# Kernel optimization log

Hardware: AMD Instinct MI355X
Metric: run time of the kernel (lower is better)

The kernel has to match this reference:

```python
import jax, jax.numpy as jnp
import numpy as np

DEFAULT_MASK_VALUE = -0.7 * float(np.finfo(np.float32).max)

B, S, HQ, HKV, D = 2, 2048, 16, 8, 128
CHUNK = 512


def _chunk_causal_mask(seq_len, chunk_size):
    # True where attention allowed: same chunk AND causal within chunk.
    row = jax.lax.broadcasted_iota(jnp.int32, (seq_len, seq_len), 0)
    col = jax.lax.broadcasted_iota(jnp.int32, (seq_len, seq_len), 1)
    return (row // chunk_size == col // chunk_size) & (row >= col)


def _block_mask_indices(bidirectional_mask):
    # [B, L] 0/1 -> segment ids, e.g. [0,1,1,1,0,0,1,1,0,1,0] -> [0,1,1,1,0,0,2,2,0,3,0]
    m = bidirectional_mask.astype(jnp.int32)
    padded = jnp.pad(m, [(0, 0), (1, 0)], constant_values=0)
    boundary = padded[..., 1:] > padded[..., :-1]
    return m * jnp.cumsum(boundary, axis=-1)


def _bidirectional_block_mask(bidirectional_mask):
    idx = _block_mask_indices(bidirectional_mask)  # [B, L]
    return (idx[:, None, :] == idx[:, :, None]) & (idx[:, :, None] > 0)  # [B, L, L]


def setup_inputs() -> dict:
    key = jax.random.key(0)
    kq, kk, kv, kb = jax.random.split(key, 4)
    q = jax.random.normal(kq, (B, S, HQ, D), dtype=jnp.float32)
    k = jax.random.normal(kk, (B, S, HKV, D), dtype=jnp.float32)
    v = jax.random.normal(kv, (B, S, HKV, D), dtype=jnp.float32)
    bidirectional_mask = jax.random.randint(kb, (B, S), 0, 2, dtype=jnp.int32)
    return {"q": q, "k": k, "v": v, "bidirectional_mask": bidirectional_mask,
            "chunk_size": CHUNK}


def reference(q, k, v, bidirectional_mask, chunk_size):
    b, s, hq, d = q.shape
    hkv = k.shape[2]
    group = hq // hkv  # GQA group size
    scale = 1.0 / jnp.sqrt(jnp.asarray(d, q.dtype))

    # [b, s, hkv, group, d]
    qg = q.reshape(b, s, hkv, group, d) * scale
    # logits: [b, hkv, group, q, kv]
    logits = jnp.einsum("bqhgd,bkhd->bhgqk", qg, k)

    # combined mask: chunked-causal OR bidirectional block (image tokens attend
    # bidirectionally within their contiguous block)
    chunk_mask = _chunk_causal_mask(s, chunk_size)                 # [s, s]
    bidir_mask = _bidirectional_block_mask(bidirectional_mask)    # [b, s, s]
    allowed = chunk_mask[None, :, :] | bidir_mask                  # [b, s, s]
    allowed = allowed[:, None, None, :, :]                         # [b, 1, 1, s, s]

    masked = jnp.where(allowed, logits, DEFAULT_MASK_VALUE)
    probs = jax.nn.softmax(masked, axis=-1)

    out = jnp.einsum("bhgqk,bkhd->bqhgd", probs, v)
    return out.reshape(b, s, hq, d)
```

## Files before the change

kernel.cpp:

```cpp
#include <hip/hip_runtime.h>
#include <hip/hip_bf16.h>

#define SLEN 2048
#define BATCH 2
#define NHQ 16
#define NHKV 8
#define DIM 128
#define SEG 512
#define NSEG (SLEN / SEG)

#define KTD (64 * 64)
#define VTD (128 * 32)

typedef __attribute__((ext_vector_type(8))) short bf16x8;
typedef __attribute__((ext_vector_type(4))) short bf16x4;
typedef __attribute__((ext_vector_type(4))) float f32x4;

static __device__ inline short f2bf(float f) {
    __hip_bfloat16 h = __float2bfloat16(f);
    return *reinterpret_cast<short*>(&h);
}
static __device__ inline unsigned pack_bf2(float lo, float hi) {
    unsigned a = (unsigned)(unsigned short)f2bf(lo);
    unsigned b = (unsigned)(unsigned short)f2bf(hi);
    return a | (b << 16);
}
static __device__ inline float fast_exp2(float x) {
#if __has_builtin(__builtin_amdgcn_exp2f)
    return __builtin_amdgcn_exp2f(x);
#else
    return __builtin_exp2f(x);
#endif
}
static __device__ inline f32x4 mfma16(bf16x4 a, bf16x4 b, f32x4 c) {
#if __has_builtin(__builtin_amdgcn_mfma_f32_16x16x16bf16_1k)
    return __builtin_amdgcn_mfma_f32_16x16x16bf16_1k(a, b, c, 0, 0, 0);
#else
    asm volatile("v_mfma_f32_16x16x16_bf16 %0, %1, %2, %0\n\ts_nop 7\n\ts_nop 7"
                 : "+v"(c) : "v"(a), "v"(b));
    return c;
#endif
}

#define GLDS(g, l) __builtin_amdgcn_global_load_lds( \
    (const __attribute__((address_space(1))) void*)(g), \
    (__attribute__((address_space(3))) void*)(l), 16, 0, 0)

__global__ __launch_bounds__(256) void conv_kv(
    const float* __restrict__ K, const float* __restrict__ V,
    unsigned short* __restrict__ Kb, unsigned short* __restrict__ Vt,
    const int* __restrict__ mask, int* __restrict__ rs, int* __restrict__ re)
{
    __shared__ float vt_s[64 * 132];
    __shared__ int   sm[SLEN];
    const int blk = blockIdx.x;
    const int NCONV = BATCH * NHKV * (SLEN / 64);

    if (blk >= NCONV) {
        const int idx = blk - NCONV;
        const int b = idx >> 3, slice = idx & 7;
        const int* mb = mask + b * SLEN;
        for (int i = threadIdx.x; i < SLEN; i += 256) sm[i] = mb[i];
        __syncthreads();
        const int i = slice * 256 + threadIdx.x;
        int s0 = -1, e0 = -2;
        if (sm[i] == 1) {
            s0 = i; while (s0 > 0 && sm[s0 - 1] == 1) --s0;
            e0 = i; while (e0 < SLEN - 1 && sm[e0 + 1] == 1) ++e0;
        }
        rs[b * SLEN + i] = s0;
        re[b * SLEN + i] = e0;
        return;
    }

    const int st = blk & 31;
    const int h  = (blk >> 5) & 7;
    const int b  = blk >> 8;
    const int s0 = st * 64;
    const int sl = threadIdx.x >> 2;
    const int dq = (threadIdx.x & 3) * 32;

    {
        const float* ksrc = K + (((size_t)(b * SLEN + s0 + sl) * NHKV + h) * DIM) + dq;
        unsigned short* kdst = Kb + (((size_t)(b * NHKV + h) * SLEN) + s0 + sl) * DIM + dq;
        #pragma unroll
        for (int i = 0; i < 4; ++i) {
            float4 a = ((const float4*)ksrc)[2 * i];
            float4 c = ((const float4*)ksrc)[2 * i + 1];
            ((uint4*)kdst)[i] = make_uint4(pack_bf2(a.x, a.y), pack_bf2(a.z, a.w),
                                           pack_bf2(c.x, c.y), pack_bf2(c.z, c.w));
        }
    }

    {
        const float* vsrc = V + (((size_t)(b * SLEN + s0 + sl) * NHKV + h) * DIM) + dq;
        float4* ld = (float4*)&vt_s[sl * 132 + dq];
        #pragma unroll
        for (int i = 0; i < 8; ++i) ld[i] = ((const float4*)vsrc)[i];
    }
    __syncthreads();
    #pragma unroll
    for (int pass = 0; pass < 2; ++pass) {
        const int dl = (threadIdx.x >> 2) + pass * 64;
        const int sw = (threadIdx.x & 3) * 16;
        unsigned pk[8];
        #pragma unroll
        for (int m = 0; m < 8; ++m)
            pk[m] = pack_bf2(vt_s[(sw + 2 * m) * 132 + dl],
                             vt_s[(sw + 2 * m + 1) * 132 + dl]);
        unsigned short* dst = Vt + (((size_t)(b * NHKV + h) * DIM) + dl) * SLEN + s0 + sw;
        ((uint4*)dst)[0] = make_uint4(pk[0], pk[1], pk[2], pk[3]);
        ((uint4*)dst)[1] = make_uint4(pk[4], pk[5], pk[6], pk[7]);
    }
}

__global__ __launch_bounds__(512, 2) void attn_fwd(
    const float* __restrict__ Q, const unsigned short* __restrict__ KbP,
    const unsigned short* __restrict__ VtP, const int* __restrict__ rs,
    const int* __restrict__ re, const int* __restrict__ csp,
    float* __restrict__ Out)
{
    const int tid  = threadIdx.x;
    const int wid  = tid >> 6;
    const int lane = tid & 63;
    const int quad = lane >> 4;
    const int n    = lane & 15;

    const int bid   = blockIdx.x;
    const int h     = bid & 7;
    const int inner = (bid >> 3) & 15;
    const int q4    = (bid >> 7) & 3;
    const int band  = (q4 == 0) ? 3 : (q4 == 1) ? 2 : (q4 == 2) ? 0 : 1;
    const int b     = inner & 1;
    const int hq    = h * 2 + ((inner >> 1) & 1);
    const int chunk = inner >> 2;
    const int r0 = chunk * SEG + band * 128 + wid * 16;

    __shared__ unsigned pool[2 * KTD + 2 * VTD];

    const float scale = 0.08838834764831845f * 1.4426950408889634f;
    const int cs = csp[0];

    const int* rsb = rs + b * SLEN;
    const int* reb = re + b * SLEN;

    const int row  = r0 + n;
    const int rsvq = rsb[row];
    const int csrq = (row / cs) * cs;
    int lo_rt, hi_rt;
    {
        const int revq = reb[row];
        int lo = csrq; if (rsvq >= 0 && rsvq < lo) lo = rsvq;
        int hi = row;  if (revq > hi) hi = revq;
        #pragma unroll
        for (int off = 8; off > 0; off >>= 1) {
            lo = min(lo, __shfl_xor(lo, off, 64));
            hi = max(hi, __shfl_xor(hi, off, 64));
        }
        lo_rt = lo; hi_rt = hi;
    }
    const int cshi = ((r0 + 15) / cs) * cs;

    bf16x8 qa[4];
    {
        const float* qp = Q + (((size_t)(b * SLEN + row) * NHQ + hq) * DIM) + quad * 8;
        #pragma unroll
        for (int kb = 0; kb < 4; ++kb) {
            float4 f0 = *(const float4*)(qp + kb * 32);
            float4 f1 = *(const float4*)(qp + kb * 32 + 4);
            bf16x8 a;
            a[0] = f2bf(f0.x * scale); a[1] = f2bf(f0.y * scale);
            a[2] = f2bf(f0.z * scale); a[3] = f2bf(f0.w * scale);
            a[4] = f2bf(f1.x * scale); a[5] = f2bf(f1.y * scale);
            a[6] = f2bf(f1.z * scale); a[7] = f2bf(f1.w * scale);
            qa[kb] = a;
        }
    }

    int lo_blk, hi_blk;
    {
        int* sred = (int*)pool;
        if (lane == 0) { sred[wid * 2] = lo_rt; sred[wid * 2 + 1] = hi_rt; }
        __syncthreads();
        int lo = 0x7fffffff, hi = 0;
        #pragma unroll
        for (int i = 0; i < 8; ++i) {
            lo = min(lo, sred[2 * i]);
            hi = max(hi, sred[2 * i + 1]);
        }
        __syncthreads();
        lo_blk = lo & ~63;
        hi_blk = hi;
    }

    float lrow = 0.0f;
    f32x4 o[8];
    #pragma unroll
    for (int nb = 0; nb < 8; ++nb) o[nb] = (f32x4){0.f, 0.f, 0.f, 0.f};

    const unsigned short* KbB = KbP + (size_t)(b * NHKV + h) * SLEN * DIM;
    const unsigned short* VtB = VtP + (size_t)(b * NHKV + h) * DIM * SLEN;

    const int kr0  = tid >> 4;
    const int ksl  = (tid & 15) ^ (kr0 & 15);
    const size_t koff = (size_t)kr0 * DIM + ksl * 8;
    const int vr0  = tid >> 3;
    const int vsl  = (tid & 7) ^ (vr0 & 7);
    const size_t voff = (size_t)vr0 * SLEN + vsl * 8;

    int rsv_c;
    {
        const unsigned short* ks = KbB + (size_t)lo_blk * DIM + koff;
        const unsigned short* vs = VtB + lo_blk + voff;
        char* kl = (char*)pool;
        char* vl = (char*)pool + 32768;
        GLDS(ks,                     kl + tid * 16);
        GLDS(ks + (size_t)32 * DIM,  kl + 8192 + tid * 16);
        GLDS(vs,                     vl + tid * 16);
        GLDS(vs + (size_t)64 * SLEN, vl + 8192 + tid * 16);
        rsv_c = rsb[lo_blk + lane];
    }
    __syncthreads();

    int bufi = 0;
    for (int k0 = lo_blk; k0 <= hi_blk; k0 += 64, bufi ^= 1) {
        int rsv_n = rsv_c;
        if (k0 + 64 <= hi_blk) {
            const int kn0 = k0 + 64;
            const unsigned short* ks = KbB + (size_t)kn0 * DIM + koff;
            const unsigned short* vs = VtB + kn0 + voff;
            char* kl = (char*)pool + (bufi ^ 1) * 16384;
            char* vl = (char*)pool + 32768 + (bufi ^ 1) * 16384;
            GLDS(ks,                     kl + tid * 16);
            GLDS(ks + (size_t)32 * DIM,  kl + 8192 + tid * 16);
            GLDS(vs,                     vl + tid * 16);
            GLDS(vs + (size_t)64 * SLEN, vl + 8192 + tid * 16);
            rsv_n = rsb[kn0 + lane];
        }

        if ((k0 + 63 >= lo_rt) && (k0 <= hi_rt)) {
            const short* ktb = (const short*)(pool + bufi * KTD);
            const short* vtb = (const short*)(pool + 2 * KTD + bufi * VTD);

            f32x4 sfr[4];
            #pragma unroll
            for (int c = 0; c < 4; ++c) sfr[c] = (f32x4){0.f, 0.f, 0.f, 0.f};
            __builtin_amdgcn_s_setprio(1);
            #pragma unroll
            for (int c = 0; c < 4; ++c) {
                #pragma unroll
                for (int kb = 0; kb < 4; ++kb) {
                    const bf16x8 kf = *(const bf16x8*)(ktb +
                        (c * 16 + n) * DIM + (((kb * 4 + quad) ^ n) * 8));
                    sfr[c] = __builtin_amdgcn_mfma_f32_16x16x32_bf16(kf, qa[kb], sfr[c], 0, 0, 0);
                }
            }
            __builtin_amdgcn_s_setprio(0);

            const bool fullc = (k0 >= cshi) && (k0 + 63 <= r0);
            if (!fullc) {
                #pragma unroll
                for (int c = 0; c < 4; ++c) {
                    #pragma unroll
                    for (int g = 0; g < 4; ++g) {
                        const int kcl  = k0 + c * 16 + quad * 4 + g;
                        const int rskv = __shfl(rsv_c, c * 16 + quad * 4 + g, 64);
                        const bool ok = ((kcl >= csrq) && (kcl <= row)) ||
                                        (rsvq >= 0 && rskv == rsvq);
                        if (!ok) sfr[c][g] = -3.0e38f;
                    }
                }
            }

            bf16x4 pa[4];
            #pragma unroll
            for (int c = 0; c < 4; ++c) {
                float p0 = fast_exp2(sfr[c][0]);
                float p1 = fast_exp2(sfr[c][1]);
                float p2 = fast_exp2(sfr[c][2]);
                float p3 = fast_exp2(sfr[c][3]);
                lrow += (p0 + p1) + (p2 + p3);
                uint2 ww = make_uint2(pack_bf2(p0, p1), pack_bf2(p2, p3));
                pa[c] = __builtin_bit_cast(bf16x4, ww);
            }

            __builtin_amdgcn_s_setprio(1);
            #pragma unroll
            for (int c = 0; c < 4; ++c) {
                #pragma unroll
                for (int nb = 0; nb < 8; ++nb) {
                    const bf16x4 vb = *(const bf16x4*)(vtb +
                        (nb * 16 + n) * 64 + (((c * 2 + (quad >> 1)) ^ (n & 7)) * 8)
                        + (quad & 1) * 4);
                    o[nb] = mfma16(pa[c], vb, o[nb]);
                }
            }
            __builtin_amdgcn_s_setprio(0);
        }

        __syncthreads();
        rsv_c = rsv_n;
    }

    lrow += __shfl_xor(lrow, 16, 64);
    lrow += __shfl_xor(lrow, 32, 64);
    const float inv = 1.0f / lrow;
    #pragma unroll
    for (int g = 0; g < 4; ++g) {
        const float invg = __shfl(inv, quad * 4 + g, 64);
        const int r = r0 + quad * 4 + g;
        float* op = Out + ((size_t)(b * SLEN + r) * NHQ + hq) * DIM + n;
        #pragma unroll
        for (int nb = 0; nb < 8; ++nb)
            op[nb * 16] = o[nb][g] * invg;
    }
}

extern "C" void kernel_launch(void* const* d_in, const int* in_sizes, int n_in,
                              void* d_out, int out_size, void* d_ws, size_t ws_size,
                              hipStream_t stream) {
    const float* q  = (const float*)d_in[0];
    const float* k  = (const float*)d_in[1];
    const float* v  = (const float*)d_in[2];
    const int*   bm = (const int*)d_in[3];
    const int*   cs = (const int*)d_in[4];
    float* out = (float*)d_out;

    int* rs = (int*)d_ws;
    int* re = rs + BATCH * SLEN;
    unsigned short* Kb = (unsigned short*)((char*)d_ws + 32768);
    unsigned short* Vt = Kb + (size_t)BATCH * NHKV * SLEN * DIM;

    hipLaunchKernelGGL(conv_kv, dim3(BATCH * NHKV * (SLEN / 64) + BATCH * 8), dim3(256),
                       0, stream, k, v, Kb, Vt, bm, rs, re);
    hipLaunchKernelGGL(attn_fwd, dim3(512), dim3(512), 0, stream,
                       q, Kb, Vt, rs, re, cs, out);
}
```

Before: 131.3 us.

## Process two 16-row query tiles per wave to reuse K/V fragments

Each wave now handles 32 query rows as two 16-row sub-tiles, so every K and V fragment read from LDS feeds two MFMAs. The block shrinks from 512 to 256 threads, and each thread issues four async global-to-LDS loads per tile instead of two. The aim is to halve LDS reads per MFMA and cut per-block overhead. The cost is roughly double the accumulator and Q registers, plus launch bounds of (256,1) that may lower occupancy and latency hiding.

```diff
diff --git a/kernel.cpp b/kernel.cpp
--- a/kernel.cpp
+++ b/kernel.cpp
@@ -114,7 +114,7 @@
     }
 }
 
-__global__ __launch_bounds__(512, 2) void attn_fwd(
+__global__ __launch_bounds__(256, 1) void attn_fwd(
     const float* __restrict__ Q, const unsigned short* __restrict__ KbP,
     const unsigned short* __restrict__ VtP, const int* __restrict__ rs,
     const int* __restrict__ re, const int* __restrict__ csp,
@@ -134,7 +134,7 @@
     const int b     = inner & 1;
     const int hq    = h * 2 + ((inner >> 1) & 1);
     const int chunk = inner >> 2;
-    const int r0 = chunk * SEG + band * 128 + wid * 16;
+    const int r0 = chunk * SEG + band * 128 + wid * 32;
 
     __shared__ unsigned pool[2 * KTD + 2 * VTD];
 
@@ -144,14 +144,20 @@
     const int* rsb = rs + b * SLEN;
     const int* reb = re + b * SLEN;
 
-    const int row  = r0 + n;
-    const int rsvq = rsb[row];
-    const int csrq = (row / cs) * cs;
+    const int row0 = r0 + n;
+    const int row1 = r0 + 16 + n;
+    const int rsv0 = rsb[row0];
+    const int rsv1 = rsb[row1];
+    const int csr0 = (row0 / cs) * cs;
+    const int csr1 = (row1 / cs) * cs;
     int lo_rt, hi_rt;
     {
-        const int revq = reb[row];
-        int lo = csrq; if (rsvq >= 0 && rsvq < lo) lo = rsvq;
-        int hi = row;  if (revq > hi) hi = revq;
+        const int rev0 = reb[row0];
+        const int rev1 = reb[row1];
+        int lo = min(csr0, csr1);
+        if (rsv0 >= 0) lo = min(lo, rsv0);
+        if (rsv1 >= 0) lo = min(lo, rsv1);
+        int hi = max(max(row1, rev0), rev1);
         #pragma unroll
         for (int off = 8; off > 0; off >>= 1) {
             lo = min(lo, __shfl_xor(lo, off, 64));
@@ -159,11 +165,13 @@
         }
         lo_rt = lo; hi_rt = hi;
     }
-    const int cshi = ((r0 + 15) / cs) * cs;
-
-    bf16x8 qa[4];
-    {
-        const float* qp = Q + (((size_t)(b * SLEN + row) * NHQ + hq) * DIM) + quad * 8;
+    const int cshi0 = ((r0 + 15) / cs) * cs;
+    const int cshi1 = ((r0 + 31) / cs) * cs;
+
+    bf16x8 qa[2][4];
+    #pragma unroll
+    for (int u = 0; u < 2; ++u) {
+        const float* qp = Q + (((size_t)(b * SLEN + r0 + 16 * u + n) * NHQ + hq) * DIM) + quad * 8;
         #pragma unroll
         for (int kb = 0; kb < 4; ++kb) {
             float4 f0 = *(const float4*)(qp + kb * 32);
@@ -173,7 +181,7 @@
             a[2] = f2bf(f0.z * scale); a[3] = f2bf(f0.w * scale);
             a[4] = f2bf(f1.x * scale); a[5] = f2bf(f1.y * scale);
             a[6] = f2bf(f1.z * scale); a[7] = f2bf(f1.w * scale);
-            qa[kb] = a;
+            qa[u][kb] = a;
         }
     }
 
@@ -184,7 +192,7 @@
         __syncthreads();
         int lo = 0x7fffffff, hi = 0;
         #pragma unroll
-        for (int i = 0; i < 8; ++i) {
+        for (int i = 0; i < 4; ++i) {
             lo = min(lo, sred[2 * i]);
             hi = max(hi, sred[2 * i + 1]);
         }
@@ -193,20 +201,20 @@
         hi_blk = hi;
     }
 
-    float lrow = 0.0f;
-    f32x4 o[8];
+    float lrow[2] = {0.f, 0.f};
+    f32x4 o[2][8];
     #pragma unroll
-    for (int nb = 0; nb < 8; ++nb) o[nb] = (f32x4){0.f, 0.f, 0.f, 0.f};
+    for (int u = 0; u < 2; ++u)
+        #pragma unroll
+        for (int nb = 0; nb < 8; ++nb) o[u][nb] = (f32x4){0.f, 0.f, 0.f, 0.f};
 
     const unsigned short* KbB = KbP + (size_t)(b * NHKV + h) * SLEN * DIM;
     const unsigned short* VtB = VtP + (size_t)(b * NHKV + h) * DIM * SLEN;
 
-    const int kr0  = tid >> 4;
-    const int ksl  = (tid & 15) ^ (kr0 & 15);
-    const size_t koff = (size_t)kr0 * DIM + ksl * 8;
-    const int vr0  = tid >> 3;
-    const int vsl  = (tid & 7) ^ (vr0 & 7);
-    const size_t voff = (size_t)vr0 * SLEN + vsl * 8;
+    const int ksl  = (tid & 15) ^ ((tid >> 4) & 15);
+    const size_t koff = (size_t)(tid >> 4) * DIM + ksl * 8;
+    const int vsl  = (tid & 7) ^ ((tid >> 3) & 7);
+    const size_t voff = (size_t)(tid >> 3) * SLEN + vsl * 8;
 
     int rsv_c;
     {
@@ -214,10 +222,11 @@
         const unsigned short* vs = VtB + lo_blk + voff;
         char* kl = (char*)pool;
         char* vl = (char*)pool + 32768;
-        GLDS(ks,                     kl + tid * 16);
-        GLDS(ks + (size_t)32 * DIM,  kl + 8192 + tid * 16);
-        GLDS(vs,                     vl + tid * 16);
-        GLDS(vs + (size_t)64 * SLEN, vl + 8192 + tid * 16);
+        #pragma unroll
+        for (int p = 0; p < 4; ++p) {
+            GLDS(ks + (size_t)(p * 16) * DIM,  kl + tid * 16 + p * 4096);
+            GLDS(vs + (size_t)(p * 32) * SLEN, vl + tid * 16 + p * 4096);
+        }
         rsv_c = rsb[lo_blk + lane];
     }
     __syncthreads();
@@ -231,10 +240,11 @@
             const unsigned short* vs = VtB + kn0 + voff;
             char* kl = (char*)pool + (bufi ^ 1) * 16384;
             char* vl = (char*)pool + 32768 + (bufi ^ 1) * 16384;
-            GLDS(ks,                     kl + tid * 16);
-            GLDS(ks + (size_t)32 * DIM,  kl + 8192 + tid * 16);
-            GLDS(vs,                     vl + tid * 16);
-            GLDS(vs + (size_t)64 * SLEN, vl + 8192 + tid * 16);
+            #pragma unroll
+            for (int p = 0; p < 4; ++p) {
+                GLDS(ks + (size_t)(p * 16) * DIM,  kl + tid * 16 + p * 4096);
+                GLDS(vs + (size_t)(p * 32) * SLEN, vl + tid * 16 + p * 4096);
+            }
             rsv_n = rsb[kn0 + lane];
         }
 
@@ -242,9 +252,11 @@
             const short* ktb = (const short*)(pool + bufi * KTD);
             const short* vtb = (const short*)(pool + 2 * KTD + bufi * VTD);
 
-            f32x4 sfr[4];
-            #pragma unroll
-            for (int c = 0; c < 4; ++c) sfr[c] = (f32x4){0.f, 0.f, 0.f, 0.f};
+            f32x4 sfr[2][4];
+            #pragma unroll
+            for (int u = 0; u < 2; ++u)
+                #pragma unroll
+                for (int c = 0; c < 4; ++c) sfr[u][c] = (f32x4){0.f, 0.f, 0.f, 0.f};
             __builtin_amdgcn_s_setprio(1);
             #pragma unroll
             for (int c = 0; c < 4; ++c) {
@@ -252,36 +264,48 @@
                 for (int kb = 0; kb < 4; ++kb) {
                     const bf16x8 kf = *(const bf16x8*)(ktb +
                         (c * 16 + n) * DIM + (((kb * 4 + quad) ^ n) * 8));
-                    sfr[c] = __builtin_amdgcn_mfma_f32_16x16x32_bf16(kf, qa[kb], sfr[c], 0, 0, 0);
+                    sfr[0][c] = __builtin_amdgcn_mfma_f32_16x16x32_bf16(kf, qa[0][kb], sfr[0][c], 0, 0, 0);
+                    sfr[1][c] = __builtin_amdgcn_mfma_f32_16x16x32_bf16(kf, qa[1][kb], sfr[1][c], 0, 0, 0);
                 }
             }
             __builtin_amdgcn_s_setprio(0);
 
-            const bool fullc = (k0 >= cshi) && (k0 + 63 <= r0);
-            if (!fullc) {
+            const bool f0 = (k0 >= cshi0) && (k0 + 63 <= r0);
+            const bool f1 = (k0 >= cshi1) && (k0 + 63 <= r0 + 16);
+            if (!(f0 && f1)) {
                 #pragma unroll
                 for (int c = 0; c < 4; ++c) {
                     #pragma unroll
                     for (int g = 0; g < 4; ++g) {
                         const int kcl  = k0 + c * 16 + quad * 4 + g;
                         const int rskv = __shfl(rsv_c, c * 16 + quad * 4 + g, 64);
-                        const bool ok = ((kcl >= csrq) && (kcl <= row)) ||
-                                        (rsvq >= 0 && rskv == rsvq);
-                        if (!ok) sfr[c][g] = -3.0e38f;
+                        if (!f0) {
+                            const bool ok = ((kcl >= csr0) && (kcl <= row0)) ||
+                                            (rsv0 >= 0 && rskv == rsv0);
+                            if (!ok) sfr[0][c][g] = -3.0e38f;
+                        }
+                        if (!f1) {
+                            const bool ok = ((kcl >= csr1) && (kcl <= row1)) ||
+                                            (rsv1 >= 0 && rskv == rsv1);
+                            if (!ok) sfr[1][c][g] = -3.0e38f;
+                        }
                     }
                 }
             }
 
-            bf16x4 pa[4];
-            #pragma unroll
-            for (int c = 0; c < 4; ++c) {
-                float p0 = fast_exp2(sfr[c][0]);
-                float p1 = fast_exp2(sfr[c][1]);
-                float p2 = fast_exp2(sfr[c][2]);
-                float p3 = fast_exp2(sfr[c][3]);
-                lrow += (p0 + p1) + (p2 + p3);
-                uint2 ww = make_uint2(pack_bf2(p0, p1), pack_bf2(p2, p3));
-                pa[c] = __builtin_bit_cast(bf16x4, ww);
+            bf16x4 pa[2][4];
+            #pragma unroll
+            for (int u = 0; u < 2; ++u) {
+                #pragma unroll
+                for (int c = 0; c < 4; ++c) {
+                    float p0 = fast_exp2(sfr[u][c][0]);
+                    float p1 = fast_exp2(sfr[u][c][1]);
+                    float p2 = fast_exp2(sfr[u][c][2]);
+                    float p3 = fast_exp2(sfr[u][c][3]);
+                    lrow[u] += (p0 + p1) + (p2 + p3);
+                    uint2 ww = make_uint2(pack_bf2(p0, p1), pack_bf2(p2, p3));
+                    pa[u][c] = __builtin_bit_cast(bf16x4, ww);
+                }
             }
 
             __builtin_amdgcn_s_setprio(1);
@@ -292,7 +316,8 @@
                     const bf16x4 vb = *(const bf16x4*)(vtb +
                         (nb * 16 + n) * 64 + (((c * 2 + (quad >> 1)) ^ (n & 7)) * 8)
                         + (quad & 1) * 4);
-                    o[nb] = mfma16(pa[c], vb, o[nb]);
+                    o[0][nb] = mfma16(pa[0][c], vb, o[0][nb]);
+                    o[1][nb] = mfma16(pa[1][c], vb, o[1][nb]);
                 }
             }
             __builtin_amdgcn_s_setprio(0);
@@ -302,17 +327,21 @@
         rsv_c = rsv_n;
     }
 
-    lrow += __shfl_xor(lrow, 16, 64);
-    lrow += __shfl_xor(lrow, 32, 64);
-    const float inv = 1.0f / lrow;
     #pragma unroll
-    for (int g = 0; g < 4; ++g) {
-        const float invg = __shfl(inv, quad * 4 + g, 64);
-        const int r = r0 + quad * 4 + g;
-        float* op = Out + ((size_t)(b * SLEN + r) * NHQ + hq) * DIM + n;
-        #pragma unroll
-        for (int nb = 0; nb < 8; ++nb)
-            op[nb * 16] = o[nb][g] * invg;
+    for (int u = 0; u < 2; ++u) {
+        float l = lrow[u];
+        l += __shfl_xor(l, 16, 64);
+        l += __shfl_xor(l, 32, 64);
+        const float inv = 1.0f / l;
+        #pragma unroll
+        for (int g = 0; g < 4; ++g) {
+            const float invg = __shfl(inv, quad * 4 + g, 64);
+            const int r = r0 + 16 * u + quad * 4 + g;
+            float* op = Out + ((size_t)(b * SLEN + r) * NHQ + hq) * DIM + n;
+            #pragma unroll
+            for (int nb = 0; nb < 8; ++nb)
+                op[nb * 16] = o[u][nb][g] * invg;
+        }
     }
 }
 
@@ -333,6 +362,6 @@
 
     hipLaunchKernelGGL(conv_kv, dim3(BATCH * NHKV * (SLEN / 64) + BATCH * 8), dim3(256),
                        0, stream, k, v, Kb, Vt, bm, rs, re);
-    hipLaunchKernelGGL(attn_fwd, dim3(512), dim3(512), 0, stream,
+    hipLaunchKernelGGL(attn_fwd, dim3(512), dim3(256), 0, stream,
                        q, Kb, Vt, rs, re, cs, out);
 }
```

Result: slower. 151.3 us (+15.2%).
